# Kernel tuning notes

Hardware: AMD Instinct MI355X
Metric: run time of the kernel (lower is better)

The kernel has to match this reference:

```python
import jax, jax.numpy as jnp
import numpy as np

N, E, D, H, O = 10000, 640000, 128, 256, 1


def setup_inputs() -> dict:
    key = jax.random.key(0)
    ks = jax.random.split(key, 10)
    s = 0.05
    return {
        "x": jax.random.normal(ks[0], (N, D), dtype=jnp.float32),
        "edge_index": jax.random.randint(ks[1], (2, E), 0, N, dtype=jnp.int64),
        # GraphConv (PyG): lin_rel (with bias) applied to sum-aggregated neighbors,
        # lin_root (no bias) applied to self features.
        "W_rel": jax.random.normal(ks[2], (D, D), dtype=jnp.float32) * s,
        "b_rel": jnp.zeros((D,), dtype=jnp.float32),
        "W_root": jax.random.normal(ks[3], (D, D), dtype=jnp.float32) * s,
        # MLP: D -> H -> H -> O, ReLU between layers
        "W1": jax.random.normal(ks[4], (H, D), dtype=jnp.float32) * s,
        "b1": jnp.zeros((H,), dtype=jnp.float32),
        "W2": jax.random.normal(ks[5], (H, H), dtype=jnp.float32) * s,
        "b2": jnp.zeros((H,), dtype=jnp.float32),
        "W3": jax.random.normal(ks[6], (O, H), dtype=jnp.float32) * s,
        "b3": jnp.zeros((O,), dtype=jnp.float32),
    }


def reference(x, edge_index, W_rel, b_rel, W_root, W1, b1, W2, b2, W3, b3):
    src, dst = edge_index[0], edge_index[1]
    # gather source features along edges, scatter-add to destinations
    agg = jax.ops.segment_sum(x[src], dst, num_segments=N)  # [N, D]
    h = agg @ W_rel.T + b_rel + x @ W_root.T                 # GraphConv out [N, D]
    h = jax.nn.relu(h @ W1.T + b1)
    h = jax.nn.relu(h @ W2.T + b2)
    h = h @ W3.T + b3                                        # [N, O]
    return jax.nn.sigmoid(h)
```

## Files before the change

kernel.cpp:

```cpp
#include <hip/hip_runtime.h>
#include <hip/hip_bf16.h>
#include <cmath>

constexpr int N_NODES = 10000;
constexpr int D_IN = 128;
constexpr int H_DIM = 256;

constexpr int NB = 313;
constexpr int BCAP = 3072;
constexpr int EPB_A = 2048;

typedef unsigned short u16;
typedef short bf16x8 __attribute__((ext_vector_type(8)));
typedef float f32x4 __attribute__((ext_vector_type(4)));

__device__ inline u16 f2bf(float f) {
    return __builtin_bit_cast(u16, __float2bfloat16(f));
}
__device__ inline float bf2f(u16 u) {
    unsigned int v = (unsigned int)u << 16;
    return __builtin_bit_cast(float, v);
}

constexpr int PREP_XB = 1250, PREP_WB = 128;
__global__ __launch_bounds__(256)
void prep_kernel(const float* __restrict__ x,
                 const float* __restrict__ W_rel, const float* __restrict__ W_root,
                 const float* __restrict__ W1, const float* __restrict__ W2,
                 u16* __restrict__ x_bf,
                 u16* __restrict__ Wcat, u16* __restrict__ W1b, u16* __restrict__ W2b,
                 int* __restrict__ gcnt) {
    const int bid = blockIdx.x, t = threadIdx.x;
    if (bid < PREP_XB) {
        int idx = bid * 256 + t;
        if (idx >= N_NODES * 32) return;
        int row = idx >> 5, c = (idx & 31) * 4;
        float4 v = *reinterpret_cast<const float4*>(x + (size_t)row * D_IN + c);
        ushort4 o;
        o.x = f2bf(v.x); o.y = f2bf(v.y); o.z = f2bf(v.z); o.w = f2bf(v.w);
        *reinterpret_cast<ushort4*>(x_bf + (size_t)row * D_IN + c) = o;
    } else if (bid < PREP_XB + PREP_WB) {
        int idx4 = ((bid - PREP_XB) * 256 + t) * 4;
        const float* src;
        u16* dst;
        if (idx4 < 32768) {
            int n = idx4 >> 8, k = idx4 & 255;
            src = (k < 128) ? W_rel + n * 128 + k : W_root + n * 128 + (k - 128);
            dst = Wcat + idx4;
        } else if (idx4 < 65536) {
            src = W1 + (idx4 - 32768);
            dst = W1b + (idx4 - 32768);
        } else {
            src = W2 + (idx4 - 65536);
            dst = W2b + (idx4 - 65536);
        }
        float4 v = *reinterpret_cast<const float4*>(src);
        ushort4 o;
        o.x = f2bf(v.x); o.y = f2bf(v.y); o.z = f2bf(v.z); o.w = f2bf(v.w);
        *reinterpret_cast<ushort4*>(dst) = o;
    } else {
        for (int i = t; i < NB; i += 256) gcnt[i] = 0;
    }
}

__global__ __launch_bounds__(256)
void binsort_a(const int* __restrict__ ei, int* __restrict__ gcnt,
               int* __restrict__ buckets, int E) {
    __shared__ int lcnt[NB], gbase[NB];
    const int t = threadIdx.x;
    for (int i = t; i < NB; i += 256) lcnt[i] = 0;
    __syncthreads();
    const int e0 = blockIdx.x * EPB_A + t;
    int packed[8], lpos[8], bb[8];
#pragma unroll
    for (int j = 0; j < 8; ++j) {
        int e = e0 + j * 256;
        if (e < E) {
            int s = ei[e], d = ei[E + e];
            int b = d >> 5;
            bb[j] = b;
            packed[j] = ((d & 31) << 16) | s;
            lpos[j] = atomicAdd(&lcnt[b], 1);
        } else bb[j] = -1;
    }
    __syncthreads();
    for (int i = t; i < NB; i += 256)
        gbase[i] = atomicAdd(&gcnt[i], lcnt[i]);
    __syncthreads();
#pragma unroll
    for (int j = 0; j < 8; ++j)
        if (bb[j] >= 0)
            buckets[bb[j] * BCAP + gbase[bb[j]] + lpos[j]] = packed[j];
}

__global__ __launch_bounds__(512)
void sortgather(const int* __restrict__ gcnt, const int* __restrict__ buckets,
                const u16* __restrict__ x_bf, u16* __restrict__ agg_bf, int M) {
    __shared__ int edges[BCAP];
    __shared__ u16 ssrc[BCAP];
    __shared__ int deg[32], cur[32], sbeg[32];
    const int b = blockIdx.x, t = threadIdx.x;
    const int w = t >> 6, lane = t & 63;
    if (t < 32) deg[t] = 0;
    __syncthreads();
    int cnt = gcnt[b]; if (cnt > BCAP) cnt = BCAP;
    for (int i = t; i < cnt; i += 512) {
        int p = buckets[b * BCAP + i];
        edges[i] = p;
        atomicAdd(&deg[p >> 16], 1);
    }
    __syncthreads();
    if (t < 32) {
        int d = deg[t];
        int incl = d;
#pragma unroll
        for (int off = 1; off < 32; off <<= 1) {
            int o = __shfl_up(incl, off);
            if (t >= off) incl += o;
        }
        int excl = incl - d;
        cur[t] = excl;
        sbeg[t] = excl;
    }
    __syncthreads();
    for (int i = t; i < cnt; i += 512) {
        int p = edges[i];
        int pos = atomicAdd(&cur[p >> 16], 1);
        ssrc[pos] = (u16)(p & 0xffff);
    }
    __syncthreads();
    const int c = (lane & 31) * 4;
    const int r = lane >> 5;
#pragma unroll
    for (int j = 0; j < 4; ++j) {
        int ln = w * 4 + j;
        int beg = sbeg[ln], dg = deg[ln];
        int half = (dg + 1) >> 1;
        int i = beg + (r ? half : 0);
        const int i1 = r ? beg + dg : beg + half;
        float4 a0 = {0, 0, 0, 0}, a1 = {0, 0, 0, 0};
        float4 a2 = {0, 0, 0, 0}, a3 = {0, 0, 0, 0};
        for (; i + 4 <= i1; i += 4) {
            int s0 = ssrc[i + 0], s1 = ssrc[i + 1];
            int s2 = ssrc[i + 2], s3 = ssrc[i + 3];
            ushort4 v0 = *reinterpret_cast<const ushort4*>(x_bf + (size_t)s0 * D_IN + c);
            ushort4 v1 = *reinterpret_cast<const ushort4*>(x_bf + (size_t)s1 * D_IN + c);
            ushort4 v2 = *reinterpret_cast<const ushort4*>(x_bf + (size_t)s2 * D_IN + c);
            ushort4 v3 = *reinterpret_cast<const ushort4*>(x_bf + (size_t)s3 * D_IN + c);
            a0.x += bf2f(v0.x); a0.y += bf2f(v0.y); a0.z += bf2f(v0.z); a0.w += bf2f(v0.w);
            a1.x += bf2f(v1.x); a1.y += bf2f(v1.y); a1.z += bf2f(v1.z); a1.w += bf2f(v1.w);
            a2.x += bf2f(v2.x); a2.y += bf2f(v2.y); a2.z += bf2f(v2.z); a2.w += bf2f(v2.w);
            a3.x += bf2f(v3.x); a3.y += bf2f(v3.y); a3.z += bf2f(v3.z); a3.w += bf2f(v3.w);
        }
        for (; i < i1; ++i) {
            int s = ssrc[i];
            ushort4 v = *reinterpret_cast<const ushort4*>(x_bf + (size_t)s * D_IN + c);
            a0.x += bf2f(v.x); a0.y += bf2f(v.y); a0.z += bf2f(v.z); a0.w += bf2f(v.w);
        }
        a0.x += a1.x + a2.x + a3.x;
        a0.y += a1.y + a2.y + a3.y;
        a0.z += a1.z + a2.z + a3.z;
        a0.w += a1.w + a2.w + a3.w;
        a0.x += __shfl_xor(a0.x, 32);
        a0.y += __shfl_xor(a0.y, 32);
        a0.z += __shfl_xor(a0.z, 32);
        a0.w += __shfl_xor(a0.w, 32);
        int node = b * 32 + ln;
        if (r == 0 && node < M) {
            ushort4 o;
            o.x = f2bf(a0.x); o.y = f2bf(a0.y); o.z = f2bf(a0.z); o.w = f2bf(a0.w);
            *reinterpret_cast<ushort4*>(agg_bf + (size_t)node * D_IN + c) = o;
        }
    }
}

__global__ __launch_bounds__(512)
void fused_mlp(const u16* __restrict__ agg_bf, const u16* __restrict__ x_bf,
               const u16* __restrict__ Wcat, const u16* __restrict__ W1b,
               const u16* __restrict__ W2b,
               const float* __restrict__ b_rel, const float* __restrict__ b1,
               const float* __restrict__ b2, const float* __restrict__ W3,
               const float* __restrict__ b3, float* __restrict__ out, int M) {
    __shared__ u16 bufA[64 * 264];
    __shared__ u16 bufH0[64 * 136];
    __shared__ u16 wbuf[34816];
    __shared__ float part[64][4];
    const int t = threadIdx.x, b = blockIdx.x;
    const int w = t >> 6, lane = t & 63;
    const int wm = w >> 2, wn = w & 3;
    const int l16 = lane & 15, q = lane >> 4;
    const int r0 = b * 64;

    for (int idx = t; idx < 64 * 16; idx += 512) {
        int row = idx >> 4, kc = (idx & 15) * 8;
        int gr = r0 + row; if (gr >= M) gr = M - 1;
        bf16x8 v = *reinterpret_cast<const bf16x8*>(agg_bf + (size_t)gr * D_IN + kc);
        *reinterpret_cast<bf16x8*>(&bufA[row * 264 + kc]) = v;
        bf16x8 vx = *reinterpret_cast<const bf16x8*>(x_bf + (size_t)gr * D_IN + kc);
        *reinterpret_cast<bf16x8*>(&bufA[row * 264 + 128 + kc]) = vx;
    }
    for (int idx = t; idx < 128 * 32; idx += 512) {
        int row = idx >> 5, kc = (idx & 31) * 8;
        bf16x8 v = *reinterpret_cast<const bf16x8*>(Wcat + (size_t)row * 256 + kc);
        *reinterpret_cast<bf16x8*>(&wbuf[row * 264 + kc]) = v;
    }
    __syncthreads();

    {
        f32x4 acc[2][2] = {};
#pragma unroll
        for (int k0 = 0; k0 < 256; k0 += 32) {
            bf16x8 af[2];
#pragma unroll
            for (int i = 0; i < 2; ++i)
                af[i] = *reinterpret_cast<const bf16x8*>(
                    &bufA[(wm * 32 + i * 16 + l16) * 264 + k0 + q * 8]);
#pragma unroll
            for (int jj = 0; jj < 2; ++jj) {
                int col = wn * 32 + jj * 16 + l16;
                bf16x8 bv = *reinterpret_cast<const bf16x8*>(
                    &wbuf[col * 264 + k0 + q * 8]);
                acc[0][jj] = __builtin_amdgcn_mfma_f32_16x16x32_bf16(af[0], bv, acc[0][jj], 0, 0, 0);
                acc[1][jj] = __builtin_amdgcn_mfma_f32_16x16x32_bf16(af[1], bv, acc[1][jj], 0, 0, 0);
            }
        }
#pragma unroll
        for (int i = 0; i < 2; ++i)
#pragma unroll
            for (int jj = 0; jj < 2; ++jj) {
                int col = wn * 32 + jj * 16 + l16;
                float bb = b_rel[col];
#pragma unroll
                for (int r = 0; r < 4; ++r) {
                    int row = wm * 32 + i * 16 + q * 4 + r;
                    bufH0[row * 136 + col] = f2bf(acc[i][jj][r] + bb);
                }
            }
    }
    __syncthreads();

    for (int idx = t; idx < 256 * 16; idx += 512) {
        int row = idx >> 4, kc = (idx & 15) * 8;
        bf16x8 v = *reinterpret_cast<const bf16x8*>(W1b + (size_t)row * 128 + kc);
        *reinterpret_cast<bf16x8*>(&wbuf[row * 136 + kc]) = v;
    }
    __syncthreads();

    {
        f32x4 acc[2][4] = {};
#pragma unroll
        for (int k0 = 0; k0 < 128; k0 += 32) {
            bf16x8 af[2];
#pragma unroll
            for (int i = 0; i < 2; ++i)
                af[i] = *reinterpret_cast<const bf16x8*>(
                    &bufH0[(wm * 32 + i * 16 + l16) * 136 + k0 + q * 8]);
#pragma unroll
            for (int jj = 0; jj < 4; ++jj) {
                int col = wn * 64 + jj * 16 + l16;
                bf16x8 bv = *reinterpret_cast<const bf16x8*>(
                    &wbuf[col * 136 + k0 + q * 8]);
                acc[0][jj] = __builtin_amdgcn_mfma_f32_16x16x32_bf16(af[0], bv, acc[0][jj], 0, 0, 0);
                acc[1][jj] = __builtin_amdgcn_mfma_f32_16x16x32_bf16(af[1], bv, acc[1][jj], 0, 0, 0);
            }
        }
#pragma unroll
        for (int i = 0; i < 2; ++i)
#pragma unroll
            for (int jj = 0; jj < 4; ++jj) {
                int col = wn * 64 + jj * 16 + l16;
                float bb = b1[col];
#pragma unroll
                for (int r = 0; r < 4; ++r) {
                    int row = wm * 32 + i * 16 + q * 4 + r;
                    bufA[row * 264 + col] = f2bf(fmaxf(acc[i][jj][r] + bb, 0.f));
                }
            }
    }

    float s[2][4] = {};
#pragma unroll
    for (int h = 0; h < 2; ++h) {
        __syncthreads();
        for (int idx = t; idx < 128 * 32; idx += 512) {
            int row = idx >> 5, kc = (idx & 31) * 8;
            bf16x8 v = *reinterpret_cast<const bf16x8*>(
                W2b + (size_t)(h * 128 + row) * 256 + kc);
            *reinterpret_cast<bf16x8*>(&wbuf[row * 264 + kc]) = v;
        }
        __syncthreads();
        f32x4 acc[2][2] = {};
#pragma unroll
        for (int k0 = 0; k0 < 256; k0 += 32) {
            bf16x8 af[2];
#pragma unroll
            for (int i = 0; i < 2; ++i)
                af[i] = *reinterpret_cast<const bf16x8*>(
                    &bufA[(wm * 32 + i * 16 + l16) * 264 + k0 + q * 8]);
#pragma unroll
            for (int jj = 0; jj < 2; ++jj) {
                int lcol = wn * 32 + jj * 16 + l16;
                bf16x8 bv = *reinterpret_cast<const bf16x8*>(
                    &wbuf[lcol * 264 + k0 + q * 8]);
                acc[0][jj] = __builtin_amdgcn_mfma_f32_16x16x32_bf16(af[0], bv, acc[0][jj], 0, 0, 0);
                acc[1][jj] = __builtin_amdgcn_mfma_f32_16x16x32_bf16(af[1], bv, acc[1][jj], 0, 0, 0);
            }
        }
#pragma unroll
        for (int jj = 0; jj < 2; ++jj) {
            int col = h * 128 + wn * 32 + jj * 16 + l16;
            float bb = b2[col], ww = W3[col];
#pragma unroll
            for (int i = 0; i < 2; ++i)
#pragma unroll
                for (int r = 0; r < 4; ++r)
                    s[i][r] = fmaf(fmaxf(acc[i][jj][r] + bb, 0.f), ww, s[i][r]);
        }
    }
#pragma unroll
    for (int off = 1; off < 16; off <<= 1)
#pragma unroll
        for (int i = 0; i < 2; ++i)
#pragma unroll
            for (int r = 0; r < 4; ++r)
                s[i][r] += __shfl_xor(s[i][r], off);
    if (l16 == 0)
#pragma unroll
        for (int i = 0; i < 2; ++i)
#pragma unroll
            for (int r = 0; r < 4; ++r)
                part[wm * 32 + i * 16 + q * 4 + r][wn] = s[i][r];
    __syncthreads();
    if (t < 64) {
        int node = r0 + t;
        if (node < M) {
            float v = part[t][0] + part[t][1] + part[t][2] + part[t][3] + b3[0];
            out[node] = 1.0f / (1.0f + expf(-v));
        }
    }
}

extern "C" void kernel_launch(void* const* d_in, const int* in_sizes, int n_in,
                              void* d_out, int out_size, void* d_ws, size_t ws_size,
                              hipStream_t stream) {
    const float* x      = (const float*)d_in[0];
    const int*   ei     = (const int*)d_in[1];
    const float* W_rel  = (const float*)d_in[2];
    const float* b_rel  = (const float*)d_in[3];
    const float* W_root = (const float*)d_in[4];
    const float* W1     = (const float*)d_in[5];
    const float* b1     = (const float*)d_in[6];
    const float* W2     = (const float*)d_in[7];
    const float* b2     = (const float*)d_in[8];
    const float* W3     = (const float*)d_in[9];
    const float* b3     = (const float*)d_in[10];
    float* out = (float*)d_out;
    const int E = in_sizes[1] / 2;

    char* p = (char*)d_ws;
    auto carve = [&](size_t bytes) { char* r = p; p += (bytes + 63) & ~size_t(63); return r; };
    u16* x_bf   = (u16*)carve((size_t)N_NODES * D_IN * 2);
    u16* agg_bf = (u16*)carve((size_t)N_NODES * D_IN * 2);
    u16* Wcat   = (u16*)carve(128 * 256 * 2);
    u16* W1b    = (u16*)carve(256 * 128 * 2);
    u16* W2b    = (u16*)carve(256 * 256 * 2);
    int* gcnt    = (int*)carve(NB * 4);
    int* buckets = (int*)carve((size_t)NB * BCAP * 4);

    prep_kernel<<<PREP_XB + PREP_WB + 1, 256, 0, stream>>>(
        x, W_rel, W_root, W1, W2, x_bf, Wcat, W1b, W2b, gcnt);
    binsort_a<<<(E + EPB_A - 1) / EPB_A, 256, 0, stream>>>(ei, gcnt, buckets, E);
    sortgather<<<NB, 512, 0, stream>>>(gcnt, buckets, x_bf, agg_bf, N_NODES);
    fused_mlp<<<(N_NODES + 63) / 64, 512, 0, stream>>>(
        agg_bf, x_bf, Wcat, W1b, W2b, b_rel, b1, b2, W3, b3, out, N_NODES);
}
```

Before: 126.5 us.

## Fuse prep, binsort, gather and MLP into one cooperative grid-synced kernel

Replaces the four-kernel pipeline with a single cooperative kernel of 157 blocks. It converts inputs to bf16 and bins edges by destination, then does one grid-wide sync. After that each block sorts two buckets in shared memory, aggregates 64 nodes straight into its MLP input tile, and runs the MLP. This removes three launch gaps and the global round trip of the aggregated features. The cost is only 157 blocks (one wave), a grid barrier, and the x_bf gather being read right after the other blocks write it. The old path stays as a fallback if the cooperative launch fails.

```diff
diff --git a/kernel.cpp b/kernel.cpp
--- a/kernel.cpp
+++ b/kernel.cpp
@@ -1,6 +1,9 @@
 #include <hip/hip_runtime.h>
 #include <hip/hip_bf16.h>
+#include <hip/hip_cooperative_groups.h>
 #include <cmath>
+
+namespace cg = cooperative_groups;
 
 constexpr int N_NODES = 10000;
 constexpr int D_IN = 128;
@@ -9,6 +12,10 @@
 constexpr int NB = 313;
 constexpr int BCAP = 3072;
 constexpr int EPB_A = 2048;
+
+constexpr int GRID = 157;
+constexpr int THREADS = 512;
+constexpr int EPB = 4096;
 
 typedef unsigned short u16;
 typedef short bf16x8 __attribute__((ext_vector_type(8)));
@@ -20,6 +27,332 @@
 __device__ inline float bf2f(u16 u) {
     unsigned int v = (unsigned int)u << 16;
     return __builtin_bit_cast(float, v);
+}
+
+__global__ __launch_bounds__(THREADS)
+void mega(const float* __restrict__ x, const int* __restrict__ ei,
+          const float* __restrict__ W_rel, const float* __restrict__ W_root,
+          const float* __restrict__ W1, const float* __restrict__ W2,
+          const float* __restrict__ b_rel, const float* __restrict__ b1,
+          const float* __restrict__ b2, const float* __restrict__ W3,
+          const float* __restrict__ b3,
+          u16* __restrict__ x_bf, u16* __restrict__ Wcat,
+          u16* __restrict__ W1b, u16* __restrict__ W2b,
+          int* __restrict__ gcnt, int* __restrict__ buckets,
+          float* __restrict__ out, int E, int M)
+{
+    __shared__ alignas(16) u16 bufA[64 * 264];
+    __shared__ alignas(16) u16 bufH0[64 * 136];
+    union alignas(16) Ovl {
+        struct { int lcnt[NB]; int gbase[NB]; } h;
+        struct { int edges[2][BCAP]; u16 ssrc[2][BCAP]; } s;
+        u16 wbuf[34816];
+    };
+    __shared__ Ovl ovl;
+    __shared__ int deg[2][32], cur[2][32], sbeg[2][32];
+    __shared__ float part[64][4];
+
+    const int t = threadIdx.x, blk = blockIdx.x;
+    const int w = t >> 6, lane = t & 63;
+    const int wm = w >> 2, wn = w & 3;
+    const int l16 = lane & 15, q = lane >> 4;
+    const int r0 = blk * 64;
+
+    {
+        const int tid = blk * THREADS + t;
+        for (int idx = tid; idx < N_NODES * 32; idx += GRID * THREADS) {
+            int row = idx >> 5, c = (idx & 31) * 4;
+            float4 v = *reinterpret_cast<const float4*>(x + (size_t)row * D_IN + c);
+            ushort4 o;
+            o.x = f2bf(v.x); o.y = f2bf(v.y); o.z = f2bf(v.z); o.w = f2bf(v.w);
+            *reinterpret_cast<ushort4*>(x_bf + (size_t)row * D_IN + c) = o;
+        }
+        if (tid < 32768) {
+            int idx4 = tid * 4;
+            const float* src;
+            u16* dst;
+            if (idx4 < 32768) {
+                int n = idx4 >> 8, k = idx4 & 255;
+                src = (k < 128) ? W_rel + n * 128 + k : W_root + n * 128 + (k - 128);
+                dst = Wcat + idx4;
+            } else if (idx4 < 65536) {
+                src = W1 + (idx4 - 32768);
+                dst = W1b + (idx4 - 32768);
+            } else {
+                src = W2 + (idx4 - 65536);
+                dst = W2b + (idx4 - 65536);
+            }
+            float4 v = *reinterpret_cast<const float4*>(src);
+            ushort4 o;
+            o.x = f2bf(v.x); o.y = f2bf(v.y); o.z = f2bf(v.z); o.w = f2bf(v.w);
+            *reinterpret_cast<ushort4*>(dst) = o;
+        }
+        for (int i = t; i < NB; i += THREADS) ovl.h.lcnt[i] = 0;
+        __syncthreads();
+        const int e0 = blk * EPB + t;
+        int packed[8], lpos[8], bb[8];
+#pragma unroll
+        for (int j = 0; j < 8; ++j) {
+            int e = e0 + j * THREADS;
+            if (e < E) {
+                int s = ei[e], d = ei[E + e];
+                int b = d >> 5;
+                bb[j] = b;
+                packed[j] = ((d & 31) << 16) | s;
+                lpos[j] = atomicAdd(&ovl.h.lcnt[b], 1);
+            } else bb[j] = -1;
+        }
+        __syncthreads();
+        for (int i = t; i < NB; i += THREADS)
+            ovl.h.gbase[i] = atomicAdd(&gcnt[i], ovl.h.lcnt[i]);
+        __syncthreads();
+#pragma unroll
+        for (int j = 0; j < 8; ++j)
+            if (bb[j] >= 0)
+                buckets[bb[j] * BCAP + ovl.h.gbase[bb[j]] + lpos[j]] = packed[j];
+    }
+
+    __threadfence();
+    cg::this_grid().sync();
+    __threadfence();
+
+    int cnt[2];
+#pragma unroll
+    for (int k = 0; k < 2; ++k) {
+        int bk = blk * 2 + k;
+        int c = (bk < NB) ? gcnt[bk] : 0;
+        cnt[k] = c > BCAP ? BCAP : c;
+    }
+    if (t < 64) deg[t >> 5][t & 31] = 0;
+    __syncthreads();
+
+    for (int idx = t; idx < 64 * 16; idx += THREADS) {
+        int row = idx >> 4, kc = (idx & 15) * 8;
+        int gr = r0 + row; if (gr >= M) gr = M - 1;
+        bf16x8 vx = *reinterpret_cast<const bf16x8*>(x_bf + (size_t)gr * D_IN + kc);
+        *reinterpret_cast<bf16x8*>(&bufA[row * 264 + 128 + kc]) = vx;
+    }
+#pragma unroll
+    for (int k = 0; k < 2; ++k) {
+        int bk = blk * 2 + k;
+        for (int i = t; i < cnt[k]; i += THREADS) {
+            int p = buckets[bk * BCAP + i];
+            ovl.s.edges[k][i] = p;
+            atomicAdd(&deg[k][p >> 16], 1);
+        }
+    }
+    __syncthreads();
+    if (t < 64) {
+        int k = t >> 5, tl = t & 31;
+        int d = deg[k][tl], incl = d;
+#pragma unroll
+        for (int off = 1; off < 32; off <<= 1) {
+            int o = __shfl_up(incl, off, 32);
+            if (tl >= off) incl += o;
+        }
+        cur[k][tl] = incl - d;
+        sbeg[k][tl] = incl - d;
+    }
+    __syncthreads();
+#pragma unroll
+    for (int k = 0; k < 2; ++k)
+        for (int i = t; i < cnt[k]; i += THREADS) {
+            int p = ovl.s.edges[k][i];
+            int pos = atomicAdd(&cur[k][p >> 16], 1);
+            ovl.s.ssrc[k][pos] = (u16)(p & 0xffff);
+        }
+    __syncthreads();
+
+    {
+        const int c4 = (lane & 31) * 4;
+        const int rh = lane >> 5;
+#pragma unroll
+        for (int k = 0; k < 2; ++k) {
+            const u16* sp = ovl.s.ssrc[k];
+#pragma unroll
+            for (int j = 0; j < 4; ++j) {
+                int ln = w * 4 + j;
+                int beg = sbeg[k][ln], dg = deg[k][ln];
+                int half = (dg + 1) >> 1;
+                int i = beg + (rh ? half : 0);
+                const int i1 = rh ? beg + dg : beg + half;
+                float4 a0 = {0, 0, 0, 0}, a1 = {0, 0, 0, 0};
+                float4 a2 = {0, 0, 0, 0}, a3 = {0, 0, 0, 0};
+                for (; i + 4 <= i1; i += 4) {
+                    int s0 = sp[i + 0], s1 = sp[i + 1];
+                    int s2 = sp[i + 2], s3 = sp[i + 3];
+                    ushort4 v0 = *reinterpret_cast<const ushort4*>(x_bf + (size_t)s0 * D_IN + c4);
+                    ushort4 v1 = *reinterpret_cast<const ushort4*>(x_bf + (size_t)s1 * D_IN + c4);
+                    ushort4 v2 = *reinterpret_cast<const ushort4*>(x_bf + (size_t)s2 * D_IN + c4);
+                    ushort4 v3 = *reinterpret_cast<const ushort4*>(x_bf + (size_t)s3 * D_IN + c4);
+                    a0.x += bf2f(v0.x); a0.y += bf2f(v0.y); a0.z += bf2f(v0.z); a0.w += bf2f(v0.w);
+                    a1.x += bf2f(v1.x); a1.y += bf2f(v1.y); a1.z += bf2f(v1.z); a1.w += bf2f(v1.w);
+                    a2.x += bf2f(v2.x); a2.y += bf2f(v2.y); a2.z += bf2f(v2.z); a2.w += bf2f(v2.w);
+                    a3.x += bf2f(v3.x); a3.y += bf2f(v3.y); a3.z += bf2f(v3.z); a3.w += bf2f(v3.w);
+                }
+                for (; i < i1; ++i) {
+                    int s = sp[i];
+                    ushort4 v = *reinterpret_cast<const ushort4*>(x_bf + (size_t)s * D_IN + c4);
+                    a0.x += bf2f(v.x); a0.y += bf2f(v.y); a0.z += bf2f(v.z); a0.w += bf2f(v.w);
+                }
+                a0.x += a1.x + a2.x + a3.x;
+                a0.y += a1.y + a2.y + a3.y;
+                a0.z += a1.z + a2.z + a3.z;
+                a0.w += a1.w + a2.w + a3.w;
+                a0.x += __shfl_xor(a0.x, 32);
+                a0.y += __shfl_xor(a0.y, 32);
+                a0.z += __shfl_xor(a0.z, 32);
+                a0.w += __shfl_xor(a0.w, 32);
+                if (rh == 0) {
+                    int row = k * 32 + ln;
+                    ushort4 o;
+                    o.x = f2bf(a0.x); o.y = f2bf(a0.y); o.z = f2bf(a0.z); o.w = f2bf(a0.w);
+                    *reinterpret_cast<ushort4*>(&bufA[row * 264 + c4]) = o;
+                }
+            }
+        }
+    }
+    __syncthreads();
+
+    for (int idx = t; idx < 128 * 32; idx += THREADS) {
+        int row = idx >> 5, kc = (idx & 31) * 8;
+        bf16x8 v = *reinterpret_cast<const bf16x8*>(Wcat + (size_t)row * 256 + kc);
+        *reinterpret_cast<bf16x8*>(&ovl.wbuf[row * 264 + kc]) = v;
+    }
+    __syncthreads();
+
+    {
+        f32x4 acc[2][2] = {};
+#pragma unroll
+        for (int k0 = 0; k0 < 256; k0 += 32) {
+            bf16x8 af[2];
+#pragma unroll
+            for (int i = 0; i < 2; ++i)
+                af[i] = *reinterpret_cast<const bf16x8*>(
+                    &bufA[(wm * 32 + i * 16 + l16) * 264 + k0 + q * 8]);
+#pragma unroll
+            for (int jj = 0; jj < 2; ++jj) {
+                int col = wn * 32 + jj * 16 + l16;
+                bf16x8 bv = *reinterpret_cast<const bf16x8*>(
+                    &ovl.wbuf[col * 264 + k0 + q * 8]);
+                acc[0][jj] = __builtin_amdgcn_mfma_f32_16x16x32_bf16(af[0], bv, acc[0][jj], 0, 0, 0);
+                acc[1][jj] = __builtin_amdgcn_mfma_f32_16x16x32_bf16(af[1], bv, acc[1][jj], 0, 0, 0);
+            }
+        }
+#pragma unroll
+        for (int i = 0; i < 2; ++i)
+#pragma unroll
+            for (int jj = 0; jj < 2; ++jj) {
+                int col = wn * 32 + jj * 16 + l16;
+                float bb = b_rel[col];
+#pragma unroll
+                for (int r = 0; r < 4; ++r) {
+                    int row = wm * 32 + i * 16 + q * 4 + r;
+                    bufH0[row * 136 + col] = f2bf(acc[i][jj][r] + bb);
+                }
+            }
+    }
+    __syncthreads();
+
+    for (int idx = t; idx < 256 * 16; idx += THREADS) {
+        int row = idx >> 4, kc = (idx & 15) * 8;
+        bf16x8 v = *reinterpret_cast<const bf16x8*>(W1b + (size_t)row * 128 + kc);
+        *reinterpret_cast<bf16x8*>(&ovl.wbuf[row * 136 + kc]) = v;
+    }
+    __syncthreads();
+
+    {
+        f32x4 acc[2][4] = {};
+#pragma unroll
+        for (int k0 = 0; k0 < 128; k0 += 32) {
+            bf16x8 af[2];
+#pragma unroll
+            for (int i = 0; i < 2; ++i)
+                af[i] = *reinterpret_cast<const bf16x8*>(
+                    &bufH0[(wm * 32 + i * 16 + l16) * 136 + k0 + q * 8]);
+#pragma unroll
+            for (int jj = 0; jj < 4; ++jj) {
+                int col = wn * 64 + jj * 16 + l16;
+                bf16x8 bv = *reinterpret_cast<const bf16x8*>(
+                    &ovl.wbuf[col * 136 + k0 + q * 8]);
+                acc[0][jj] = __builtin_amdgcn_mfma_f32_16x16x32_bf16(af[0], bv, acc[0][jj], 0, 0, 0);
+                acc[1][jj] = __builtin_amdgcn_mfma_f32_16x16x32_bf16(af[1], bv, acc[1][jj], 0, 0, 0);
+            }
+        }
+#pragma unroll
+        for (int i = 0; i < 2; ++i)
+#pragma unroll
+            for (int jj = 0; jj < 4; ++jj) {
+                int col = wn * 64 + jj * 16 + l16;
+                float bb = b1[col];
+#pragma unroll
+                for (int r = 0; r < 4; ++r) {
+                    int row = wm * 32 + i * 16 + q * 4 + r;
+                    bufA[row * 264 + col] = f2bf(fmaxf(acc[i][jj][r] + bb, 0.f));
+                }
+            }
+    }
+
+    float s[2][4] = {};
+#pragma unroll
+    for (int h = 0; h < 2; ++h) {
+        __syncthreads();
+        for (int idx = t; idx < 128 * 32; idx += THREADS) {
+            int row = idx >> 5, kc = (idx & 31) * 8;
+            bf16x8 v = *reinterpret_cast<const bf16x8*>(
+                W2b + (size_t)(h * 128 + row) * 256 + kc);
+            *reinterpret_cast<bf16x8*>(&ovl.wbuf[row * 264 + kc]) = v;
+        }
+        __syncthreads();
+        f32x4 acc[2][2] = {};
+#pragma unroll
+        for (int k0 = 0; k0 < 256; k0 += 32) {
+            bf16x8 af[2];
+#pragma unroll
+            for (int i = 0; i < 2; ++i)
+                af[i] = *reinterpret_cast<const bf16x8*>(
+                    &bufA[(wm * 32 + i * 16 + l16) * 264 + k0 + q * 8]);
+#pragma unroll
+            for (int jj = 0; jj < 2; ++jj) {
+                int lcol = wn * 32 + jj * 16 + l16;
+                bf16x8 bv = *reinterpret_cast<const bf16x8*>(
+                    &ovl.wbuf[lcol * 264 + k0 + q * 8]);
+                acc[0][jj] = __builtin_amdgcn_mfma_f32_16x16x32_bf16(af[0], bv, acc[0][jj], 0, 0, 0);
+                acc[1][jj] = __builtin_amdgcn_mfma_f32_16x16x32_bf16(af[1], bv, acc[1][jj], 0, 0, 0);
+            }
+        }
+#pragma unroll
+        for (int jj = 0; jj < 2; ++jj) {
+            int col = h * 128 + wn * 32 + jj * 16 + l16;
+            float bb = b2[col], ww = W3[col];
+#pragma unroll
+            for (int i = 0; i < 2; ++i)
+#pragma unroll
+                for (int r = 0; r < 4; ++r)
+                    s[i][r] = fmaf(fmaxf(acc[i][jj][r] + bb, 0.f), ww, s[i][r]);
+        }
+    }
+#pragma unroll
+    for (int off = 1; off < 16; off <<= 1)
+#pragma unroll
+        for (int i = 0; i < 2; ++i)
+#pragma unroll
+            for (int r = 0; r < 4; ++r)
+                s[i][r] += __shfl_xor(s[i][r], off);
+    if (l16 == 0)
+#pragma unroll
+        for (int i = 0; i < 2; ++i)
+#pragma unroll
+            for (int r = 0; r < 4; ++r)
+                part[wm * 32 + i * 16 + q * 4 + r][wn] = s[i][r];
+    __syncthreads();
+    if (t < 64) {
+        int node = r0 + t;
+        if (node < M) {
+            float v = part[t][0] + part[t][1] + part[t][2] + part[t][3] + b3[0];
+            out[node] = 1.0f / (1.0f + expf(-v));
+        }
+    }
 }
 
 constexpr int PREP_XB = 1250, PREP_WB = 128;
@@ -190,7 +523,6 @@
     const int wm = w >> 2, wn = w & 3;
     const int l16 = lane & 15, q = lane >> 4;
     const int r0 = b * 64;
-
     for (int idx = t; idx < 64 * 16; idx += 512) {
         int row = idx >> 4, kc = (idx & 15) * 8;
         int gr = r0 + row; if (gr >= M) gr = M - 1;
@@ -205,7 +537,6 @@
         *reinterpret_cast<bf16x8*>(&wbuf[row * 264 + kc]) = v;
     }
     __syncthreads();
-
     {
         f32x4 acc[2][2] = {};
 #pragma unroll
@@ -238,14 +569,12 @@
             }
     }
     __syncthreads();
-
     for (int idx = t; idx < 256 * 16; idx += 512) {
         int row = idx >> 4, kc = (idx & 15) * 8;
         bf16x8 v = *reinterpret_cast<const bf16x8*>(W1b + (size_t)row * 128 + kc);
         *reinterpret_cast<bf16x8*>(&wbuf[row * 136 + kc]) = v;
     }
     __syncthreads();
-
     {
         f32x4 acc[2][4] = {};
 #pragma unroll
@@ -277,7 +606,6 @@
                 }
             }
     }
-
     float s[2][4] = {};
 #pragma unroll
     for (int h = 0; h < 2; ++h) {
@@ -355,7 +683,8 @@
     const float* W3     = (const float*)d_in[9];
     const float* b3     = (const float*)d_in[10];
     float* out = (float*)d_out;
-    const int E = in_sizes[1] / 2;
+    int E = in_sizes[1] / 2;
+    int M = N_NODES;
 
     char* p = (char*)d_ws;
     auto carve = [&](size_t bytes) { char* r = p; p += (bytes + 63) & ~size_t(63); return r; };
@@ -367,10 +696,19 @@
     int* gcnt    = (int*)carve(NB * 4);
     int* buckets = (int*)carve((size_t)NB * BCAP * 4);
 
-    prep_kernel<<<PREP_XB + PREP_WB + 1, 256, 0, stream>>>(
-        x, W_rel, W_root, W1, W2, x_bf, Wcat, W1b, W2b, gcnt);
-    binsort_a<<<(E + EPB_A - 1) / EPB_A, 256, 0, stream>>>(ei, gcnt, buckets, E);
-    sortgather<<<NB, 512, 0, stream>>>(gcnt, buckets, x_bf, agg_bf, N_NODES);
-    fused_mlp<<<(N_NODES + 63) / 64, 512, 0, stream>>>(
-        agg_bf, x_bf, Wcat, W1b, W2b, b_rel, b1, b2, W3, b3, out, N_NODES);
+    hipMemsetAsync(gcnt, 0, NB * sizeof(int), stream);
+
+    void* args[] = { &x, &ei, &W_rel, &W_root, &W1, &W2, &b_rel, &b1, &b2, &W3, &b3,
+                     &x_bf, &Wcat, &W1b, &W2b, &gcnt, &buckets, &out, &E, &M };
+    hipError_t err = hipLaunchCooperativeKernel(
+        reinterpret_cast<const void*>(&mega), dim3(GRID), dim3(THREADS),
+        args, 0u, stream);
+    if (err != hipSuccess) {
+        prep_kernel<<<PREP_XB + PREP_WB + 1, 256, 0, stream>>>(
+            x, W_rel, W_root, W1, W2, x_bf, Wcat, W1b, W2b, gcnt);
+        binsort_a<<<(E + EPB_A - 1) / EPB_A, 256, 0, stream>>>(ei, gcnt, buckets, E);
+        sortgather<<<NB, 512, 0, stream>>>(gcnt, buckets, x_bf, agg_bf, N_NODES);
+        fused_mlp<<<(N_NODES + 63) / 64, 512, 0, stream>>>(
+            agg_bf, x_bf, Wcat, W1b, W2b, b_rel, b1, b2, W3, b3, out, N_NODES);
+    }
 }
```

Measured after the change: 240.5 us. 1.9x slower.

## Fuse prep with binning and sort-gather with the MLP into two kernels

Applied to the files above, without the earlier changes.

Merges the bf16 conversion kernel with the edge-binning kernel, and clears the bucket counters with a memset instead. It also fuses the per-bucket sort and gather with the MLP: each 1024-thread block handles two 32-node buckets and writes the aggregated rows straight into shared memory. This removes the global agg_bf round-trip and two kernel launches. In exchange the fused kernel runs only 157 blocks, so fewer CUs do the latency-bound gather, and half the waves sit idle during the MFMA phases.

```diff
diff --git a/kernel.cpp b/kernel.cpp
--- a/kernel.cpp
+++ b/kernel.cpp
@@ -9,6 +9,9 @@
 constexpr int NB = 313;
 constexpr int BCAP = 3072;
 constexpr int EPB_A = 2048;
+constexpr int K1_GRID = 313;
+constexpr int K2_GRID = 157;
+constexpr int K2_THREADS = 1024;
 
 typedef unsigned short u16;
 typedef short bf16x8 __attribute__((ext_vector_type(8)));
@@ -22,25 +25,29 @@
     return __builtin_bit_cast(float, v);
 }
 
-constexpr int PREP_XB = 1250, PREP_WB = 128;
 __global__ __launch_bounds__(256)
-void prep_kernel(const float* __restrict__ x,
-                 const float* __restrict__ W_rel, const float* __restrict__ W_root,
-                 const float* __restrict__ W1, const float* __restrict__ W2,
-                 u16* __restrict__ x_bf,
-                 u16* __restrict__ Wcat, u16* __restrict__ W1b, u16* __restrict__ W2b,
-                 int* __restrict__ gcnt) {
-    const int bid = blockIdx.x, t = threadIdx.x;
-    if (bid < PREP_XB) {
-        int idx = bid * 256 + t;
-        if (idx >= N_NODES * 32) return;
+void prep_binsort(const float* __restrict__ x, const int* __restrict__ ei,
+                  const float* __restrict__ W_rel, const float* __restrict__ W_root,
+                  const float* __restrict__ W1, const float* __restrict__ W2,
+                  u16* __restrict__ x_bf, u16* __restrict__ Wcat,
+                  u16* __restrict__ W1b, u16* __restrict__ W2b,
+                  int* __restrict__ gcnt, int* __restrict__ buckets, int E)
+{
+    __shared__ int lcnt[NB], gbase[NB];
+    const int t = threadIdx.x, blk = blockIdx.x;
+    const int tid = blk * 256 + t;
+
+    for (int i = t; i < NB; i += 256) lcnt[i] = 0;
+
+    for (int idx = tid; idx < N_NODES * 32; idx += K1_GRID * 256) {
         int row = idx >> 5, c = (idx & 31) * 4;
         float4 v = *reinterpret_cast<const float4*>(x + (size_t)row * D_IN + c);
         ushort4 o;
         o.x = f2bf(v.x); o.y = f2bf(v.y); o.z = f2bf(v.z); o.w = f2bf(v.w);
         *reinterpret_cast<ushort4*>(x_bf + (size_t)row * D_IN + c) = o;
-    } else if (bid < PREP_XB + PREP_WB) {
-        int idx4 = ((bid - PREP_XB) * 256 + t) * 4;
+    }
+    if (tid < 32768) {
+        int idx4 = tid * 4;
         const float* src;
         u16* dst;
         if (idx4 < 32768) {
@@ -58,19 +65,10 @@
         ushort4 o;
         o.x = f2bf(v.x); o.y = f2bf(v.y); o.z = f2bf(v.z); o.w = f2bf(v.w);
         *reinterpret_cast<ushort4*>(dst) = o;
-    } else {
-        for (int i = t; i < NB; i += 256) gcnt[i] = 0;
-    }
-}
-
-__global__ __launch_bounds__(256)
-void binsort_a(const int* __restrict__ ei, int* __restrict__ gcnt,
-               int* __restrict__ buckets, int E) {
-    __shared__ int lcnt[NB], gbase[NB];
-    const int t = threadIdx.x;
-    for (int i = t; i < NB; i += 256) lcnt[i] = 0;
-    __syncthreads();
-    const int e0 = blockIdx.x * EPB_A + t;
+    }
+    __syncthreads();
+
+    const int e0 = blk * EPB_A + t;
     int packed[8], lpos[8], bb[8];
 #pragma unroll
     for (int j = 0; j < 8; ++j) {
@@ -93,120 +91,134 @@
             buckets[bb[j] * BCAP + gbase[bb[j]] + lpos[j]] = packed[j];
 }
 
-__global__ __launch_bounds__(512)
-void sortgather(const int* __restrict__ gcnt, const int* __restrict__ buckets,
-                const u16* __restrict__ x_bf, u16* __restrict__ agg_bf, int M) {
-    __shared__ int edges[BCAP];
-    __shared__ u16 ssrc[BCAP];
-    __shared__ int deg[32], cur[32], sbeg[32];
-    const int b = blockIdx.x, t = threadIdx.x;
+__global__ __launch_bounds__(K2_THREADS)
+void sortgather_mlp(const int* __restrict__ gcnt, const int* __restrict__ buckets,
+                    const u16* __restrict__ x_bf,
+                    const u16* __restrict__ Wcat, const u16* __restrict__ W1b,
+                    const u16* __restrict__ W2b,
+                    const float* __restrict__ b_rel, const float* __restrict__ b1,
+                    const float* __restrict__ b2, const float* __restrict__ W3,
+                    const float* __restrict__ b3, float* __restrict__ out, int M)
+{
+    __shared__ alignas(16) u16 bufA[64 * 264];
+    __shared__ alignas(16) u16 bufH0[64 * 136];
+    union alignas(16) Ovl {
+        struct { int edges[2][BCAP]; u16 ssrc[2][BCAP]; } s;
+        u16 wbuf[34816];
+    };
+    __shared__ Ovl ovl;
+    __shared__ int deg[2][32], cur[2][32], sbeg[2][32];
+    __shared__ float part[64][4];
+
+    const int t = threadIdx.x, blk = blockIdx.x;
     const int w = t >> 6, lane = t & 63;
-    if (t < 32) deg[t] = 0;
-    __syncthreads();
-    int cnt = gcnt[b]; if (cnt > BCAP) cnt = BCAP;
-    for (int i = t; i < cnt; i += 512) {
-        int p = buckets[b * BCAP + i];
-        edges[i] = p;
-        atomicAdd(&deg[p >> 16], 1);
-    }
-    __syncthreads();
-    if (t < 32) {
-        int d = deg[t];
-        int incl = d;
-#pragma unroll
-        for (int off = 1; off < 32; off <<= 1) {
-            int o = __shfl_up(incl, off);
-            if (t >= off) incl += o;
-        }
-        int excl = incl - d;
-        cur[t] = excl;
-        sbeg[t] = excl;
-    }
-    __syncthreads();
-    for (int i = t; i < cnt; i += 512) {
-        int p = edges[i];
-        int pos = atomicAdd(&cur[p >> 16], 1);
-        ssrc[pos] = (u16)(p & 0xffff);
-    }
-    __syncthreads();
-    const int c = (lane & 31) * 4;
-    const int r = lane >> 5;
-#pragma unroll
-    for (int j = 0; j < 4; ++j) {
-        int ln = w * 4 + j;
-        int beg = sbeg[ln], dg = deg[ln];
-        int half = (dg + 1) >> 1;
-        int i = beg + (r ? half : 0);
-        const int i1 = r ? beg + dg : beg + half;
-        float4 a0 = {0, 0, 0, 0}, a1 = {0, 0, 0, 0};
-        float4 a2 = {0, 0, 0, 0}, a3 = {0, 0, 0, 0};
-        for (; i + 4 <= i1; i += 4) {
-            int s0 = ssrc[i + 0], s1 = ssrc[i + 1];
-            int s2 = ssrc[i + 2], s3 = ssrc[i + 3];
-            ushort4 v0 = *reinterpret_cast<const ushort4*>(x_bf + (size_t)s0 * D_IN + c);
-            ushort4 v1 = *reinterpret_cast<const ushort4*>(x_bf + (size_t)s1 * D_IN + c);
-            ushort4 v2 = *reinterpret_cast<const ushort4*>(x_bf + (size_t)s2 * D_IN + c);
-            ushort4 v3 = *reinterpret_cast<const ushort4*>(x_bf + (size_t)s3 * D_IN + c);
-            a0.x += bf2f(v0.x); a0.y += bf2f(v0.y); a0.z += bf2f(v0.z); a0.w += bf2f(v0.w);
-            a1.x += bf2f(v1.x); a1.y += bf2f(v1.y); a1.z += bf2f(v1.z); a1.w += bf2f(v1.w);
-            a2.x += bf2f(v2.x); a2.y += bf2f(v2.y); a2.z += bf2f(v2.z); a2.w += bf2f(v2.w);
-            a3.x += bf2f(v3.x); a3.y += bf2f(v3.y); a3.z += bf2f(v3.z); a3.w += bf2f(v3.w);
-        }
-        for (; i < i1; ++i) {
-            int s = ssrc[i];
-            ushort4 v = *reinterpret_cast<const ushort4*>(x_bf + (size_t)s * D_IN + c);
-            a0.x += bf2f(v.x); a0.y += bf2f(v.y); a0.z += bf2f(v.z); a0.w += bf2f(v.w);
-        }
-        a0.x += a1.x + a2.x + a3.x;
-        a0.y += a1.y + a2.y + a3.y;
-        a0.z += a1.z + a2.z + a3.z;
-        a0.w += a1.w + a2.w + a3.w;
-        a0.x += __shfl_xor(a0.x, 32);
-        a0.y += __shfl_xor(a0.y, 32);
-        a0.z += __shfl_xor(a0.z, 32);
-        a0.w += __shfl_xor(a0.w, 32);
-        int node = b * 32 + ln;
-        if (r == 0 && node < M) {
-            ushort4 o;
-            o.x = f2bf(a0.x); o.y = f2bf(a0.y); o.z = f2bf(a0.z); o.w = f2bf(a0.w);
-            *reinterpret_cast<ushort4*>(agg_bf + (size_t)node * D_IN + c) = o;
-        }
-    }
-}
-
-__global__ __launch_bounds__(512)
-void fused_mlp(const u16* __restrict__ agg_bf, const u16* __restrict__ x_bf,
-               const u16* __restrict__ Wcat, const u16* __restrict__ W1b,
-               const u16* __restrict__ W2b,
-               const float* __restrict__ b_rel, const float* __restrict__ b1,
-               const float* __restrict__ b2, const float* __restrict__ W3,
-               const float* __restrict__ b3, float* __restrict__ out, int M) {
-    __shared__ u16 bufA[64 * 264];
-    __shared__ u16 bufH0[64 * 136];
-    __shared__ u16 wbuf[34816];
-    __shared__ float part[64][4];
-    const int t = threadIdx.x, b = blockIdx.x;
-    const int w = t >> 6, lane = t & 63;
-    const int wm = w >> 2, wn = w & 3;
+    const int wm = (w >> 2) & 1, wn = w & 3;
     const int l16 = lane & 15, q = lane >> 4;
-    const int r0 = b * 64;
-
-    for (int idx = t; idx < 64 * 16; idx += 512) {
+    const int r0 = blk * 64;
+
+    int cnt[2];
+#pragma unroll
+    for (int k = 0; k < 2; ++k) {
+        int bk = blk * 2 + k;
+        int c = (bk < NB) ? gcnt[bk] : 0;
+        cnt[k] = c > BCAP ? BCAP : c;
+    }
+    if (t < 64) deg[t >> 5][t & 31] = 0;
+    __syncthreads();
+
+    for (int idx = t; idx < 64 * 16; idx += K2_THREADS) {
         int row = idx >> 4, kc = (idx & 15) * 8;
         int gr = r0 + row; if (gr >= M) gr = M - 1;
-        bf16x8 v = *reinterpret_cast<const bf16x8*>(agg_bf + (size_t)gr * D_IN + kc);
-        *reinterpret_cast<bf16x8*>(&bufA[row * 264 + kc]) = v;
         bf16x8 vx = *reinterpret_cast<const bf16x8*>(x_bf + (size_t)gr * D_IN + kc);
         *reinterpret_cast<bf16x8*>(&bufA[row * 264 + 128 + kc]) = vx;
     }
-    for (int idx = t; idx < 128 * 32; idx += 512) {
+#pragma unroll
+    for (int k = 0; k < 2; ++k) {
+        int bk = blk * 2 + k;
+        for (int i = t; i < cnt[k]; i += K2_THREADS) {
+            int p = buckets[bk * BCAP + i];
+            ovl.s.edges[k][i] = p;
+            atomicAdd(&deg[k][p >> 16], 1);
+        }
+    }
+    __syncthreads();
+    if (t < 64) {
+        int k = t >> 5, tl = t & 31;
+        int d = deg[k][tl], incl = d;
+#pragma unroll
+        for (int off = 1; off < 32; off <<= 1) {
+            int o = __shfl_up(incl, off, 32);
+            if (tl >= off) incl += o;
+        }
+        cur[k][tl] = incl - d;
+        sbeg[k][tl] = incl - d;
+    }
+    __syncthreads();
+#pragma unroll
+    for (int k = 0; k < 2; ++k)
+        for (int i = t; i < cnt[k]; i += K2_THREADS) {
+            int p = ovl.s.edges[k][i];
+            int pos = atomicAdd(&cur[k][p >> 16], 1);
+            ovl.s.ssrc[k][pos] = (u16)(p & 0xffff);
+        }
+    __syncthreads();
+
+    {
+        const int c4 = (lane & 31) * 4;
+        const int rh = lane >> 5;
+#pragma unroll
+        for (int j = 0; j < 4; ++j) {
+            int ln = w * 4 + j;
+            int k = ln >> 5, lnn = ln & 31;
+            const u16* sp = ovl.s.ssrc[k];
+            int beg = sbeg[k][lnn], dg = deg[k][lnn];
+            int half = (dg + 1) >> 1;
+            int i = beg + (rh ? half : 0);
+            const int i1 = rh ? beg + dg : beg + half;
+            float4 a0 = {0, 0, 0, 0}, a1 = {0, 0, 0, 0};
+            float4 a2 = {0, 0, 0, 0}, a3 = {0, 0, 0, 0};
+            for (; i + 4 <= i1; i += 4) {
+                int s0 = sp[i + 0], s1 = sp[i + 1];
+                int s2 = sp[i + 2], s3 = sp[i + 3];
+                ushort4 v0 = *reinterpret_cast<const ushort4*>(x_bf + (size_t)s0 * D_IN + c4);
+                ushort4 v1 = *reinterpret_cast<const ushort4*>(x_bf + (size_t)s1 * D_IN + c4);
+                ushort4 v2 = *reinterpret_cast<const ushort4*>(x_bf + (size_t)s2 * D_IN + c4);
+                ushort4 v3 = *reinterpret_cast<const ushort4*>(x_bf + (size_t)s3 * D_IN + c4);
+                a0.x += bf2f(v0.x); a0.y += bf2f(v0.y); a0.z += bf2f(v0.z); a0.w += bf2f(v0.w);
+                a1.x += bf2f(v1.x); a1.y += bf2f(v1.y); a1.z += bf2f(v1.z); a1.w += bf2f(v1.w);
+                a2.x += bf2f(v2.x); a2.y += bf2f(v2.y); a2.z += bf2f(v2.z); a2.w += bf2f(v2.w);
+                a3.x += bf2f(v3.x); a3.y += bf2f(v3.y); a3.z += bf2f(v3.z); a3.w += bf2f(v3.w);
+            }
+            for (; i < i1; ++i) {
+                int s = sp[i];
+                ushort4 v = *reinterpret_cast<const ushort4*>(x_bf + (size_t)s * D_IN + c4);
+                a0.x += bf2f(v.x); a0.y += bf2f(v.y); a0.z += bf2f(v.z); a0.w += bf2f(v.w);
+            }
+            a0.x += a1.x + a2.x + a3.x;
+            a0.y += a1.y + a2.y + a3.y;
+            a0.z += a1.z + a2.z + a3.z;
+            a0.w += a1.w + a2.w + a3.w;
+            a0.x += __shfl_xor(a0.x, 32);
+            a0.y += __shfl_xor(a0.y, 32);
+            a0.z += __shfl_xor(a0.z, 32);
+            a0.w += __shfl_xor(a0.w, 32);
+            if (rh == 0) {
+                ushort4 o;
+                o.x = f2bf(a0.x); o.y = f2bf(a0.y); o.z = f2bf(a0.z); o.w = f2bf(a0.w);
+                *reinterpret_cast<ushort4*>(&bufA[ln * 264 + c4]) = o;
+            }
+        }
+    }
+    __syncthreads();
+
+    for (int idx = t; idx < 128 * 32; idx += K2_THREADS) {
         int row = idx >> 5, kc = (idx & 31) * 8;
         bf16x8 v = *reinterpret_cast<const bf16x8*>(Wcat + (size_t)row * 256 + kc);
-        *reinterpret_cast<bf16x8*>(&wbuf[row * 264 + kc]) = v;
-    }
-    __syncthreads();
-
-    {
+        *reinterpret_cast<bf16x8*>(&ovl.wbuf[row * 264 + kc]) = v;
+    }
+    __syncthreads();
+
+    if (w < 8) {
         f32x4 acc[2][2] = {};
 #pragma unroll
         for (int k0 = 0; k0 < 256; k0 += 32) {
@@ -219,7 +231,7 @@
             for (int jj = 0; jj < 2; ++jj) {
                 int col = wn * 32 + jj * 16 + l16;
                 bf16x8 bv = *reinterpret_cast<const bf16x8*>(
-                    &wbuf[col * 264 + k0 + q * 8]);
+                    &ovl.wbuf[col * 264 + k0 + q * 8]);
                 acc[0][jj] = __builtin_amdgcn_mfma_f32_16x16x32_bf16(af[0], bv, acc[0][jj], 0, 0, 0);
                 acc[1][jj] = __builtin_amdgcn_mfma_f32_16x16x32_bf16(af[1], bv, acc[1][jj], 0, 0, 0);
             }
@@ -239,14 +251,14 @@
     }
     __syncthreads();
 
-    for (int idx = t; idx < 256 * 16; idx += 512) {
+    for (int idx = t; idx < 256 * 16; idx += K2_THREADS) {
         int row = idx >> 4, kc = (idx & 15) * 8;
         bf16x8 v = *reinterpret_cast<const bf16x8*>(W1b + (size_t)row * 128 + kc);
-        *reinterpret_cast<bf16x8*>(&wbuf[row * 136 + kc]) = v;
-    }
-    __syncthreads();
-
-    {
+        *reinterpret_cast<bf16x8*>(&ovl.wbuf[row * 136 + kc]) = v;
+    }
+    __syncthreads();
+
+    if (w < 8) {
         f32x4 acc[2][4] = {};
 #pragma unroll
         for (int k0 = 0; k0 < 128; k0 += 32) {
@@ -259,7 +271,7 @@
             for (int jj = 0; jj < 4; ++jj) {
                 int col = wn * 64 + jj * 16 + l16;
                 bf16x8 bv = *reinterpret_cast<const bf16x8*>(
-                    &wbuf[col * 136 + k0 + q * 8]);
+                    &ovl.wbuf[col * 136 + k0 + q * 8]);
                 acc[0][jj] = __builtin_amdgcn_mfma_f32_16x16x32_bf16(af[0], bv, acc[0][jj], 0, 0, 0);
                 acc[1][jj] = __builtin_amdgcn_mfma_f32_16x16x32_bf16(af[1], bv, acc[1][jj], 0, 0, 0);
             }
@@ -282,54 +294,58 @@
 #pragma unroll
     for (int h = 0; h < 2; ++h) {
         __syncthreads();
-        for (int idx = t; idx < 128 * 32; idx += 512) {
+        for (int idx = t; idx < 128 * 32; idx += K2_THREADS) {
             int row = idx >> 5, kc = (idx & 31) * 8;
             bf16x8 v = *reinterpret_cast<const bf16x8*>(
                 W2b + (size_t)(h * 128 + row) * 256 + kc);
-            *reinterpret_cast<bf16x8*>(&wbuf[row * 264 + kc]) = v;
+            *reinterpret_cast<bf16x8*>(&ovl.wbuf[row * 264 + kc]) = v;
         }
         __syncthreads();
-        f32x4 acc[2][2] = {};
-#pragma unroll
-        for (int k0 = 0; k0 < 256; k0 += 32) {
-            bf16x8 af[2];
+        if (w < 8) {
+            f32x4 acc[2][2] = {};
+#pragma unroll
+            for (int k0 = 0; k0 < 256; k0 += 32) {
+                bf16x8 af[2];
+#pragma unroll
+                for (int i = 0; i < 2; ++i)
+                    af[i] = *reinterpret_cast<const bf16x8*>(
+                        &bufA[(wm * 32 + i * 16 + l16) * 264 + k0 + q * 8]);
+#pragma unroll
+                for (int jj = 0; jj < 2; ++jj) {
+                    int lcol = wn * 32 + jj * 16 + l16;
+                    bf16x8 bv = *reinterpret_cast<const bf16x8*>(
+                        &ovl.wbuf[lcol * 264 + k0 + q * 8]);
+                    acc[0][jj] = __builtin_amdgcn_mfma_f32_16x16x32_bf16(af[0], bv, acc[0][jj], 0, 0, 0);
+                    acc[1][jj] = __builtin_amdgcn_mfma_f32_16x16x32_bf16(af[1], bv, acc[1][jj], 0, 0, 0);
+                }
+            }
+#pragma unroll
+            for (int jj = 0; jj < 2; ++jj) {
+                int col = h * 128 + wn * 32 + jj * 16 + l16;
+                float bb = b2[col], ww = W3[col];
+#pragma unroll
+                for (int i = 0; i < 2; ++i)
+#pragma unroll
+                    for (int r = 0; r < 4; ++r)
+                        s[i][r] = fmaf(fmaxf(acc[i][jj][r] + bb, 0.f), ww, s[i][r]);
+            }
+        }
+    }
+    if (w < 8) {
+#pragma unroll
+        for (int off = 1; off < 16; off <<= 1)
 #pragma unroll
             for (int i = 0; i < 2; ++i)
-                af[i] = *reinterpret_cast<const bf16x8*>(
-                    &bufA[(wm * 32 + i * 16 + l16) * 264 + k0 + q * 8]);
-#pragma unroll
-            for (int jj = 0; jj < 2; ++jj) {
-                int lcol = wn * 32 + jj * 16 + l16;
-                bf16x8 bv = *reinterpret_cast<const bf16x8*>(
-                    &wbuf[lcol * 264 + k0 + q * 8]);
-                acc[0][jj] = __builtin_amdgcn_mfma_f32_16x16x32_bf16(af[0], bv, acc[0][jj], 0, 0, 0);
-                acc[1][jj] = __builtin_amdgcn_mfma_f32_16x16x32_bf16(af[1], bv, acc[1][jj], 0, 0, 0);
-            }
-        }
-#pragma unroll
-        for (int jj = 0; jj < 2; ++jj) {
-            int col = h * 128 + wn * 32 + jj * 16 + l16;
-            float bb = b2[col], ww = W3[col];
+#pragma unroll
+                for (int r = 0; r < 4; ++r)
+                    s[i][r] += __shfl_xor(s[i][r], off);
+        if (l16 == 0)
 #pragma unroll
             for (int i = 0; i < 2; ++i)
 #pragma unroll
                 for (int r = 0; r < 4; ++r)
-                    s[i][r] = fmaf(fmaxf(acc[i][jj][r] + bb, 0.f), ww, s[i][r]);
-        }
-    }
-#pragma unroll
-    for (int off = 1; off < 16; off <<= 1)
-#pragma unroll
-        for (int i = 0; i < 2; ++i)
-#pragma unroll
-            for (int r = 0; r < 4; ++r)
-                s[i][r] += __shfl_xor(s[i][r], off);
-    if (l16 == 0)
-#pragma unroll
-        for (int i = 0; i < 2; ++i)
-#pragma unroll
-            for (int r = 0; r < 4; ++r)
-                part[wm * 32 + i * 16 + q * 4 + r][wn] = s[i][r];
+                    part[wm * 32 + i * 16 + q * 4 + r][wn] = s[i][r];
+    }
     __syncthreads();
     if (t < 64) {
         int node = r0 + t;
@@ -360,17 +376,15 @@
     char* p = (char*)d_ws;
     auto carve = [&](size_t bytes) { char* r = p; p += (bytes + 63) & ~size_t(63); return r; };
     u16* x_bf   = (u16*)carve((size_t)N_NODES * D_IN * 2);
-    u16* agg_bf = (u16*)carve((size_t)N_NODES * D_IN * 2);
     u16* Wcat   = (u16*)carve(128 * 256 * 2);
     u16* W1b    = (u16*)carve(256 * 128 * 2);
     u16* W2b    = (u16*)carve(256 * 256 * 2);
     int* gcnt    = (int*)carve(NB * 4);
     int* buckets = (int*)carve((size_t)NB * BCAP * 4);
 
-    prep_kernel<<<PREP_XB + PREP_WB + 1, 256, 0, stream>>>(
-        x, W_rel, W_root, W1, W2, x_bf, Wcat, W1b, W2b, gcnt);
-    binsort_a<<<(E + EPB_A - 1) / EPB_A, 256, 0, stream>>>(ei, gcnt, buckets, E);
-    sortgather<<<NB, 512, 0, stream>>>(gcnt, buckets, x_bf, agg_bf, N_NODES);
-    fused_mlp<<<(N_NODES + 63) / 64, 512, 0, stream>>>(
-        agg_bf, x_bf, Wcat, W1b, W2b, b_rel, b1, b2, W3, b3, out, N_NODES);
-}
+    hipMemsetAsync(gcnt, 0, NB * sizeof(int), stream);
+    prep_binsort<<<K1_GRID, 256, 0, stream>>>(
+        x, ei, W_rel, W_root, W1, W2, x_bf, Wcat, W1b, W2b, gcnt, buckets, E);
+    sortgather_mlp<<<K2_GRID, K2_THREADS, 0, stream>>>(
+        gcnt, buckets, x_bf, Wcat, W1b, W2b, b_rel, b1, b2, W3, b3, out, N_NODES);
+}
```

Measured after the change: 125.4 us (median of 2 runs). Within noise of the previous version (-0.9%).
